# Optimization experiments

Hardware: AMD Instinct MI355X
Metric: run time of the kernel (lower is better)

Reference implementation:

```python
import jax, jax.numpy as jnp
import numpy as np

INPUT_DIM = 768
OUTPUT_DIM = 768
GRID_SIZE = 5
BATCH = 8192


def setup_inputs() -> dict:
    key = jax.random.key(0)
    k1, k2 = jax.random.split(key)
    x = jax.random.normal(k1, (BATCH, INPUT_DIM), dtype=jnp.float32)
    coeffs = jax.random.normal(k2, (INPUT_DIM, OUTPUT_DIM, GRID_SIZE), dtype=jnp.float32) * 0.1
    scale = jnp.ones((INPUT_DIM, OUTPUT_DIM), dtype=jnp.float32)
    shift = jnp.zeros((INPUT_DIM, OUTPUT_DIM), dtype=jnp.float32)
    return {"x": x, "coeffs": coeffs, "scale": scale, "shift": shift}


def reference(x, coeffs, scale, shift):
    # x: [B, I]; coeffs: [I, J, G]; scale/shift: [I, J]
    grid = jnp.linspace(-1.0, 1.0, GRID_SIZE, dtype=x.dtype)        # [G]
    x_norm = jnp.tanh(x)                                            # [B, I]
    # RBF basis: exp(-5 * (x_norm - grid)^2) -> [B, I, G]
    basis = jnp.exp(-5.0 * (x_norm[:, :, None] - grid) ** 2)
    # Fold scale into coeffs, contract over input dim and grid:
    # out[b,j] = sum_{i,g} basis[b,i,g] * coeffs[i,j,g] * scale[i,j] + sum_i shift[i,j]
    w = coeffs * scale[:, :, None]                                  # [I, J, G]
    out = jnp.einsum('big,ijg->bj', basis, w)                       # [B, J]
    out = out + jnp.sum(shift, axis=0)                              # broadcast bias [J]
    return out
```

## Files before the change

kernel.cpp:

```cpp
#include <hip/hip_runtime.h>
#include <hip/hip_bf16.h>
#include <cstdint>
#include <cstddef>

#define BATCH 8192
#define IDIM  768
#define JDIM  768
#define GRID  5
#define KDIM  (IDIM * GRID)


__device__ __forceinline__ unsigned short f2bf(float f) {
    unsigned int u = __float_as_uint(f);
    u += 0x7fffu + ((u >> 16) & 1u);
    return (unsigned short)(u >> 16);
}

typedef __bf16 bf16x8 __attribute__((ext_vector_type(8)));
typedef float  f32x4  __attribute__((ext_vector_type(4)));
typedef unsigned short ushortx4 __attribute__((ext_vector_type(4)));

__device__ __forceinline__ void async_copy16(const void* gsrc, void* ldsdst) {
    __builtin_amdgcn_global_load_lds(
        (const __attribute__((address_space(1))) unsigned int*)gsrc,
        (__attribute__((address_space(3))) unsigned int*)ldsdst,
        16, 0, 0);
}


#define WT_I 32
#define WT_J 64
#define NJF  (JDIM / 16)
#define NKS  (KDIM / 32)

__global__ __launch_bounds__(256)
void wt_bias_kernel(const float* __restrict__ coeffs,
                    const float* __restrict__ scale,
                    const float* __restrict__ shift,
                    unsigned short* __restrict__ Wt3,
                    float* __restrict__ bias) {
    __shared__ __align__(16) unsigned short tile[GRID][WT_J][WT_I + 4];
    __shared__ float red[4][WT_J];
    const int t  = threadIdx.x;
    const int i0 = (blockIdx.x / (JDIM / WT_J)) * WT_I;
    const int j0 = (blockIdx.x % (JDIM / WT_J)) * WT_J;
    const int jj = t & 63;

    float ssum = 0.f;
#pragma unroll
    for (int it = 0; it < (WT_I * WT_J) / 256; ++it) {
        const int ii = it * 4 + (t >> 6);
        const int i = i0 + ii, j = j0 + jj;
        const float* cp = &coeffs[((size_t)i * JDIM + j) * GRID];
        const float  sc = scale[(size_t)i * JDIM + j];
        ssum += shift[(size_t)i * JDIM + j];
#pragma unroll
        for (int g = 0; g < GRID; ++g)
            tile[g][jj][ii] = f2bf(cp[g] * sc);
    }
    red[t >> 6][jj] = ssum;
    __syncthreads();
    if (t < WT_J)
        atomicAdd(&bias[j0 + t], red[0][t] + red[1][t] + red[2][t] + red[3][t]);

#pragma unroll
    for (int it = 0; it < 10; ++it) {
        const int s    = it * 256 + t;
        const int h    = s & 1;
        const int lane = (s >> 1) & 63;
        const int q    = s >> 7;
        const int jf_l = q & 3;
        const int g    = q >> 2;
        const int i_loc = (lane >> 4) * 8 + h * 4;
        const int j_loc = jf_l * 16 + (lane & 15);
        ushortx4 v = *(const ushortx4*)&tile[g][j_loc][i_loc];
        const int ks  = g * (IDIM / 32) + (i0 >> 5);
        const int jfg = (j0 >> 4) + jf_l;
        *(ushortx4*)&Wt3[((((size_t)ks * NJF + jfg) * 64 + lane) * 8) + h * 4] = v;
    }
}


__global__ __launch_bounds__(256)
void basis_kernel(const float* __restrict__ x, unsigned short* __restrict__ Abas) {
    const int idx = blockIdx.x * 256 + threadIdx.x;
    const int b  = idx / (IDIM / 4);
    const int i4 = (idx - b * (IDIM / 4)) * 4;
    const float4 xv = *(const float4*)&x[(size_t)b * IDIM + i4];
    const float xs[4] = {xv.x, xv.y, xv.z, xv.w};
    float tv[4];
#pragma unroll
    for (int u = 0; u < 4; ++u) {
        const float e = __expf(2.f * xs[u]);
        tv[u] = 1.f - 2.f / (e + 1.f);
    }
#pragma unroll
    for (int g = 0; g < GRID; ++g) {
        const float gv = -1.f + 0.5f * (float)g;
        ushortx4 o;
#pragma unroll
        for (int u = 0; u < 4; ++u) {
            const float d = tv[u] - gv;
            o[u] = f2bf(__expf(-5.f * d * d));
        }
        *(ushortx4*)&Abas[(size_t)b * KDIM + g * IDIM + i4] = o;
    }
}


#define BM 128
#define BN 96
#define BK 64
#define KT (KDIM / BK)

__global__ __launch_bounds__(256, 2)
void kan_gemm(const unsigned short* __restrict__ Abas,
              const unsigned short* __restrict__ Wt3,
              const float* __restrict__ bias,
              float* __restrict__ out) {
    __shared__ unsigned short As[3][BM * BK];

    const int t    = threadIdx.x;
    const int lane = t & 63;
    const int wave = t >> 6;
    const int m0 = blockIdx.x * BM;
    const int n0 = blockIdx.y * BN;
    const int wm = (wave >> 1) * 64;
    const int wn = (wave & 1) * 48;

    f32x4 acc[4][3] = {};

    const int lrow = t >> 3;
    const int lc   = t & 7;
    const int cg   = lc ^ (lrow & 7);
    const int ldsoff = lrow * BK + lc * 8;
    const size_t abase = (size_t)(m0 + lrow) * KDIM + cg * 8;

    auto stage_a = [&](int buf, int kt_el) {
#pragma unroll
        for (int s = 0; s < 4; ++s)
            async_copy16(&Abas[abase + (size_t)(32 * s) * KDIM + kt_el],
                         &As[buf][ldsoff + 32 * s * BK]);
    };

    const unsigned short* bp0 = Wt3 + (((size_t)((n0 + wn) >> 4) * 64 + lane) * 8);
    auto load_b = [&](int tt, bf16x8 (&dst)[6]) {
        const unsigned short* bp = bp0 + (size_t)(tt * 2) * (NJF * 512);
#pragma unroll
        for (int ks = 0; ks < 2; ++ks)
#pragma unroll
            for (int f = 0; f < 3; ++f)
                dst[ks * 3 + f] = *(const bf16x8*)&bp[(size_t)ks * (NJF * 512) + f * 512];
    };

    auto compute_tile = [&](int ab, const bf16x8 (&bfr)[6]) {
#pragma unroll
        for (int ks = 0; ks < 2; ++ks) {
            const int pc = ((ks * 4) + (lane >> 4)) ^ (lane & 7);
            bf16x8 af[4];
#pragma unroll
            for (int f = 0; f < 4; ++f)
                af[f] = *(const bf16x8*)&As[ab][(wm + f * 16 + (lane & 15)) * BK + pc * 8];
#pragma unroll
            for (int fm = 0; fm < 4; ++fm)
#pragma unroll
                for (int fn = 0; fn < 3; ++fn)
                    acc[fm][fn] = __builtin_amdgcn_mfma_f32_16x16x32_bf16(
                        af[fm], bfr[ks * 3 + fn], acc[fm][fn], 0, 0, 0);
        }
    };

    bf16x8 b0[6], b1[6];

    stage_a(0, 0);
    stage_a(1, BK);
    load_b(0, b0);

    int ac = 0, a2 = 2;
#pragma unroll 1
    for (int p = 0; p < (KT - 2) / 2; ++p) {
        int tt = 2 * p;
        stage_a(a2, (tt + 2) * BK);
        load_b(tt + 1, b1);
        asm volatile("s_waitcnt vmcnt(10)" ::: "memory");
        __builtin_amdgcn_s_barrier();
        __builtin_amdgcn_sched_barrier(0);
        compute_tile(ac, b0);
        __builtin_amdgcn_s_barrier();
        ac = (ac == 2) ? 0 : ac + 1;
        a2 = (a2 == 2) ? 0 : a2 + 1;
        ++tt;
        stage_a(a2, (tt + 2) * BK);
        load_b(tt + 1, b0);
        asm volatile("s_waitcnt vmcnt(10)" ::: "memory");
        __builtin_amdgcn_s_barrier();
        __builtin_amdgcn_sched_barrier(0);
        compute_tile(ac, b1);
        __builtin_amdgcn_s_barrier();
        ac = (ac == 2) ? 0 : ac + 1;
        a2 = (a2 == 2) ? 0 : a2 + 1;
    }
    {
        load_b(KT - 1, b1);
        asm volatile("s_waitcnt vmcnt(6)" ::: "memory");
        __builtin_amdgcn_s_barrier();
        __builtin_amdgcn_sched_barrier(0);
        compute_tile(ac, b0);
        __builtin_amdgcn_s_barrier();
        ac = (ac == 2) ? 0 : ac + 1;
    }
    {
        asm volatile("s_waitcnt vmcnt(0)" ::: "memory");
        __builtin_amdgcn_s_barrier();
        __builtin_amdgcn_sched_barrier(0);
        compute_tile(ac, b1);
    }

    const int col   = lane & 15;
    const int rbase = (lane >> 4) * 4;
#pragma unroll
    for (int fm = 0; fm < 4; ++fm) {
#pragma unroll
        for (int fn = 0; fn < 3; ++fn) {
            const int j  = n0 + wn + fn * 16 + col;
            const float bj = bias[j];
#pragma unroll
            for (int r = 0; r < 4; ++r) {
                const int row = m0 + wm + fm * 16 + rbase + r;
                out[(size_t)row * JDIM + j] = acc[fm][fn][r] + bj;
            }
        }
    }
}


__global__ __launch_bounds__(256)
void fallback_kernel(const float* __restrict__ x,
                     const float* __restrict__ coeffs,
                     const float* __restrict__ scale,
                     const float* __restrict__ shift,
                     float* __restrict__ out) {
    __shared__ float bas[KDIM];
    const int b = blockIdx.x;
    const int t = threadIdx.x;
    for (int i = t; i < IDIM; i += 256) {
        float tv = tanhf(x[(size_t)b * IDIM + i]);
#pragma unroll
        for (int g = 0; g < GRID; ++g) {
            float d = tv - (-1.0f + 0.5f * (float)g);
            bas[g * IDIM + i] = __expf(-5.0f * d * d);
        }
    }
    __syncthreads();
#pragma unroll
    for (int jj = 0; jj < 3; ++jj) {
        const int j = t + jj * 256;
        float acc = 0.f;
        for (int i = 0; i < IDIM; ++i) {
            const float sc = scale[(size_t)i * JDIM + j];
            const float* cp = &coeffs[((size_t)i * JDIM + j) * GRID];
            float s5 = 0.f;
#pragma unroll
            for (int g = 0; g < GRID; ++g) s5 += bas[g * IDIM + i] * cp[g];
            acc += s5 * sc + shift[(size_t)i * JDIM + j];
        }
        out[(size_t)b * JDIM + j] = acc;
    }
}


extern "C" void kernel_launch(void* const* d_in, const int* in_sizes, int n_in,
                              void* d_out, int out_size, void* d_ws, size_t ws_size,
                              hipStream_t stream) {
    const float* x      = (const float*)d_in[0];
    const float* coeffs = (const float*)d_in[1];
    const float* scale  = (const float*)d_in[2];
    const float* shift  = (const float*)d_in[3];
    float* out = (float*)d_out;

    const size_t wt_bytes   = (size_t)JDIM * KDIM * sizeof(unsigned short);
    const size_t bias_off   = wt_bytes;
    const size_t bias_bytes = (size_t)JDIM * sizeof(float);
    const size_t bas_off    = bias_off + bias_bytes;
    const size_t bas_bytes  = (size_t)BATCH * KDIM * sizeof(unsigned short);
    const size_t need       = bas_off + bas_bytes;

    if (ws_size >= need) {
        unsigned short* Wt3  = (unsigned short*)d_ws;
        float*          bias = (float*)((char*)d_ws + bias_off);
        unsigned short* Abas = (unsigned short*)((char*)d_ws + bas_off);

        hipMemsetAsync(bias, 0, bias_bytes, stream);
        wt_bias_kernel<<<(IDIM / WT_I) * (JDIM / WT_J), 256, 0, stream>>>(coeffs, scale, shift, Wt3, bias);
        basis_kernel<<<(BATCH * (IDIM / 4)) / 256, 256, 0, stream>>>(x, Abas);
        kan_gemm<<<dim3(BATCH / BM, JDIM / BN), 256, 0, stream>>>(Abas, Wt3, bias, out);
    } else {
        fallback_kernel<<<BATCH, 256, 0, stream>>>(x, coeffs, scale, shift, out);
    }
}
```

Before: 152.8 us.

## Merge weight-prep and basis kernels into one launch, drop bias memset

```diff
diff --git a/kernel.cpp b/kernel.cpp
--- a/kernel.cpp
+++ b/kernel.cpp
@@ -19,6 +19,7 @@
 typedef __bf16 bf16x8 __attribute__((ext_vector_type(8)));
 typedef float  f32x4  __attribute__((ext_vector_type(4)));
 typedef unsigned short ushortx4 __attribute__((ext_vector_type(4)));
+typedef unsigned short ushortx8 __attribute__((ext_vector_type(8)));
 
 __device__ __forceinline__ void async_copy16(const void* gsrc, void* ldsdst) {
     __builtin_amdgcn_global_load_lds(
@@ -32,78 +33,87 @@
 #define WT_J 64
 #define NJF  (JDIM / 16)
 #define NKS  (KDIM / 32)
+#define WT_BLOCKS  ((IDIM / WT_I) * (JDIM / WT_J))
+#define BAS_BLOCKS ((BATCH * (IDIM / 8)) / 256)
 
 __global__ __launch_bounds__(256)
-void wt_bias_kernel(const float* __restrict__ coeffs,
-                    const float* __restrict__ scale,
-                    const float* __restrict__ shift,
-                    unsigned short* __restrict__ Wt3,
-                    float* __restrict__ bias) {
-    __shared__ __align__(16) unsigned short tile[GRID][WT_J][WT_I + 4];
-    __shared__ float red[4][WT_J];
-    const int t  = threadIdx.x;
-    const int i0 = (blockIdx.x / (JDIM / WT_J)) * WT_I;
-    const int j0 = (blockIdx.x % (JDIM / WT_J)) * WT_J;
-    const int jj = t & 63;
-
-    float ssum = 0.f;
-#pragma unroll
-    for (int it = 0; it < (WT_I * WT_J) / 256; ++it) {
-        const int ii = it * 4 + (t >> 6);
-        const int i = i0 + ii, j = j0 + jj;
-        const float* cp = &coeffs[((size_t)i * JDIM + j) * GRID];
-        const float  sc = scale[(size_t)i * JDIM + j];
-        ssum += shift[(size_t)i * JDIM + j];
-#pragma unroll
-        for (int g = 0; g < GRID; ++g)
-            tile[g][jj][ii] = f2bf(cp[g] * sc);
-    }
-    red[t >> 6][jj] = ssum;
-    __syncthreads();
-    if (t < WT_J)
-        atomicAdd(&bias[j0 + t], red[0][t] + red[1][t] + red[2][t] + red[3][t]);
-
-#pragma unroll
-    for (int it = 0; it < 10; ++it) {
-        const int s    = it * 256 + t;
-        const int h    = s & 1;
-        const int lane = (s >> 1) & 63;
-        const int q    = s >> 7;
-        const int jf_l = q & 3;
-        const int g    = q >> 2;
-        const int i_loc = (lane >> 4) * 8 + h * 4;
-        const int j_loc = jf_l * 16 + (lane & 15);
-        ushortx4 v = *(const ushortx4*)&tile[g][j_loc][i_loc];
-        const int ks  = g * (IDIM / 32) + (i0 >> 5);
-        const int jfg = (j0 >> 4) + jf_l;
-        *(ushortx4*)&Wt3[((((size_t)ks * NJF + jfg) * 64 + lane) * 8) + h * 4] = v;
-    }
-}
-
-
-__global__ __launch_bounds__(256)
-void basis_kernel(const float* __restrict__ x, unsigned short* __restrict__ Abas) {
-    const int idx = blockIdx.x * 256 + threadIdx.x;
-    const int b  = idx / (IDIM / 4);
-    const int i4 = (idx - b * (IDIM / 4)) * 4;
-    const float4 xv = *(const float4*)&x[(size_t)b * IDIM + i4];
-    const float xs[4] = {xv.x, xv.y, xv.z, xv.w};
-    float tv[4];
-#pragma unroll
-    for (int u = 0; u < 4; ++u) {
-        const float e = __expf(2.f * xs[u]);
-        tv[u] = 1.f - 2.f / (e + 1.f);
-    }
-#pragma unroll
-    for (int g = 0; g < GRID; ++g) {
-        const float gv = -1.f + 0.5f * (float)g;
-        ushortx4 o;
-#pragma unroll
-        for (int u = 0; u < 4; ++u) {
-            const float d = tv[u] - gv;
-            o[u] = f2bf(__expf(-5.f * d * d));
-        }
-        *(ushortx4*)&Abas[(size_t)b * KDIM + g * IDIM + i4] = o;
+void prep_kernel(const float* __restrict__ x,
+                 const float* __restrict__ coeffs,
+                 const float* __restrict__ scale,
+                 const float* __restrict__ shift,
+                 unsigned short* __restrict__ Wt3,
+                 unsigned short* __restrict__ Abas,
+                 float* __restrict__ bias) {
+    const int bx = blockIdx.x;
+    if (bx < WT_BLOCKS) {
+        __shared__ __align__(16) unsigned short tile[GRID][WT_J][WT_I + 4];
+        __shared__ float red[4][WT_J];
+        const int t  = threadIdx.x;
+        const int i0 = (bx / (JDIM / WT_J)) * WT_I;
+        const int j0 = (bx % (JDIM / WT_J)) * WT_J;
+        const int jj = t & 63;
+
+        if (bx < (JDIM / WT_J)) {
+            float s = 0.f;
+            for (int i = (t >> 6); i < IDIM; i += 4)
+                s += shift[(size_t)i * JDIM + j0 + jj];
+            red[t >> 6][jj] = s;
+            __syncthreads();
+            if (t < WT_J)
+                bias[j0 + t] = red[0][t] + red[1][t] + red[2][t] + red[3][t];
+        }
+
+#pragma unroll
+        for (int it = 0; it < (WT_I * WT_J) / 256; ++it) {
+            const int ii = it * 4 + (t >> 6);
+            const int i = i0 + ii, j = j0 + jj;
+            const float* cp = &coeffs[((size_t)i * JDIM + j) * GRID];
+            const float  sc = scale[(size_t)i * JDIM + j];
+#pragma unroll
+            for (int g = 0; g < GRID; ++g)
+                tile[g][jj][ii] = f2bf(cp[g] * sc);
+        }
+        __syncthreads();
+
+#pragma unroll
+        for (int it = 0; it < 10; ++it) {
+            const int s    = it * 256 + t;
+            const int h    = s & 1;
+            const int lane = (s >> 1) & 63;
+            const int q    = s >> 7;
+            const int jf_l = q & 3;
+            const int g    = q >> 2;
+            const int i_loc = (lane >> 4) * 8 + h * 4;
+            const int j_loc = jf_l * 16 + (lane & 15);
+            ushortx4 v = *(const ushortx4*)&tile[g][j_loc][i_loc];
+            const int ks  = g * (IDIM / 32) + (i0 >> 5);
+            const int jfg = (j0 >> 4) + jf_l;
+            *(ushortx4*)&Wt3[((((size_t)ks * NJF + jfg) * 64 + lane) * 8) + h * 4] = v;
+        }
+    } else {
+        const int idx = (bx - WT_BLOCKS) * 256 + threadIdx.x;
+        const int b  = idx / (IDIM / 8);
+        const int i8 = (idx - b * (IDIM / 8)) * 8;
+        const float4 xv0 = *(const float4*)&x[(size_t)b * IDIM + i8];
+        const float4 xv1 = *(const float4*)&x[(size_t)b * IDIM + i8 + 4];
+        const float xs[8] = {xv0.x, xv0.y, xv0.z, xv0.w, xv1.x, xv1.y, xv1.z, xv1.w};
+        float tv[8];
+#pragma unroll
+        for (int u = 0; u < 8; ++u) {
+            const float e = __expf(2.f * xs[u]);
+            tv[u] = 1.f - 2.f / (e + 1.f);
+        }
+#pragma unroll
+        for (int g = 0; g < GRID; ++g) {
+            const float gv = -1.f + 0.5f * (float)g;
+            ushortx8 o;
+#pragma unroll
+            for (int u = 0; u < 8; ++u) {
+                const float d = tv[u] - gv;
+                o[u] = f2bf(__expf(-5.f * d * d));
+            }
+            *(ushortx8*)&Abas[(size_t)b * KDIM + g * IDIM + i8] = o;
+        }
     }
 }
 
@@ -290,9 +300,8 @@
         float*          bias = (float*)((char*)d_ws + bias_off);
         unsigned short* Abas = (unsigned short*)((char*)d_ws + bas_off);
 
-        hipMemsetAsync(bias, 0, bias_bytes, stream);
-        wt_bias_kernel<<<(IDIM / WT_I) * (JDIM / WT_J), 256, 0, stream>>>(coeffs, scale, shift, Wt3, bias);
-        basis_kernel<<<(BATCH * (IDIM / 4)) / 256, 256, 0, stream>>>(x, Abas);
+        prep_kernel<<<WT_BLOCKS + BAS_BLOCKS, 256, 0, stream>>>(
+            x, coeffs, scale, shift, Wt3, Abas, bias);
         kan_gemm<<<dim3(BATCH / BM, JDIM / BN), 256, 0, stream>>>(Abas, Wt3, bias, out);
     } else {
         fallback_kernel<<<BATCH, 256, 0, stream>>>(x, coeffs, scale, shift, out);
```

New measurement: 190.6 us. 1.25x slower.
